# Optimization experiments

Measured on AMD Instinct MI355X. Metric: run time of the kernel, lower is better.

## Reference

```python
import jax, jax.numpy as jnp
import numpy as np
from jax import lax

B, P, DMAX, DMEL, H = 32, 192, 48, 80, 64
BN_EPS = 1e-5


def setup_inputs() -> dict:
    key = jax.random.key(0)
    ks = jax.random.split(key, 20)
    T = P * DMAX
    s = 0.1
    k_gru = 1.0 / np.sqrt(H)
    inp = {
        "mels": jax.random.normal(ks[0], (B, T, DMEL), jnp.float32),
        # phone durations in frames, in [1, DMAX]
        "durations": jax.random.randint(ks[1], (B, P), 0, DMAX, dtype=jnp.int32) + 1,
        "max_dur": DMAX,
        "conv_w": 1.0 + s * jax.random.normal(ks[2], (2,), jnp.float32),
        "conv_b": s * jax.random.normal(ks[3], (2,), jnp.float32),
        "bn_gamma": 0.5 + jax.random.uniform(ks[4], (2,), jnp.float32),
        "bn_beta": s * jax.random.normal(ks[5], (2,), jnp.float32),
        "bn_mean": s * jax.random.normal(ks[6], (2,), jnp.float32),
        "bn_var": 0.5 + jax.random.uniform(ks[7], (2,), jnp.float32),
        "W_ih_f": k_gru * jax.random.normal(ks[8], (3 * H, DMEL), jnp.float32),
        "W_hh_f": k_gru * jax.random.normal(ks[9], (3 * H, H), jnp.float32),
        "b_ih_f": k_gru * jax.random.normal(ks[10], (3 * H,), jnp.float32),
        "b_hh_f": k_gru * jax.random.normal(ks[11], (3 * H,), jnp.float32),
        "W_ih_b": k_gru * jax.random.normal(ks[12], (3 * H, DMEL), jnp.float32),
        "W_hh_b": k_gru * jax.random.normal(ks[13], (3 * H, H), jnp.float32),
        "b_ih_b": k_gru * jax.random.normal(ks[14], (3 * H,), jnp.float32),
        "b_hh_b": k_gru * jax.random.normal(ks[15], (3 * H,), jnp.float32),
    }
    return inp


def gru_cell(x, h, Wih, Whh, bih, bhh):
    # PyTorch GRU cell convention (gate order r, z, n)
    gi = x @ Wih.T + bih
    gh = h @ Whh.T + bhh
    ir, iz, inn = jnp.split(gi, 3, axis=-1)
    hr, hz, hn = jnp.split(gh, 3, axis=-1)
    r = jax.nn.sigmoid(ir + hr)
    z = jax.nn.sigmoid(iz + hz)
    n = jnp.tanh(inn + r * hn)
    return (1.0 - z) * n + z * h


def reference(mels, durations, max_dur, conv_w, conv_b, bn_gamma, bn_beta,
              bn_mean, bn_var, W_ih_f, W_hh_f, b_ih_f, b_hh_f,
              W_ih_b, W_hh_b, b_ih_b, b_hh_b):
    Bq, T, D = mels.shape
    Pq = durations.shape[1]
    Hq = W_hh_f.shape[1]

    # --- mel2phone: gather each phone's mel segment into [B, P, DMAX, D] ---
    ends = jnp.cumsum(durations, axis=1)
    starts = ends - durations
    t = jnp.arange(max_dur)
    idx = jnp.clip(starts[:, :, None] + t[None, None, :], 0, T - 1)  # [B,P,Dmax]
    segs = mels[jnp.arange(Bq)[:, None, None], idx]                  # [B,P,Dmax,D]
    mask = t[None, None, :] < durations[:, :, None]                  # [B,P,Dmax]

    # --- ConvBNorms2d: 1x1 single-channel conv + eval-mode BN + ReLU, x n_layers ---
    x = segs
    for i in range(conv_w.shape[0]):
        x = conv_w[i] * x + conv_b[i]
        x = (x - bn_mean[i]) * (bn_gamma[i] / jnp.sqrt(bn_var[i] + BN_EPS)) + bn_beta[i]
        x = jax.nn.relu(x)

    # --- per-segment bidirectional GRU, keep last valid timestep ---
    BP = Bq * Pq
    xs = x.reshape(BP, max_dur, D).transpose(1, 0, 2)        # [Dmax, BP, D]
    ms = mask.reshape(BP, max_dur).T                         # [Dmax, BP]

    def step(h, inp):
        xt, mt = inp
        hn = gru_cell(xt, h, W_ih_f, W_hh_f, b_ih_f, b_hh_f)
        h = jnp.where(mt[:, None], hn, h)  # freeze hidden past segment end
        return h, None

    h0 = jnp.zeros((BP, Hq), x.dtype)
    h_fwd, _ = lax.scan(step, h0, (xs, ms))                  # fwd hidden at len-1

    # backward direction output at the last valid position = one GRU step on x[len-1]
    last_idx = jnp.clip(durations - 1, 0, max_dur - 1)       # [B,P]
    x_last = jnp.take_along_axis(x, last_idx[:, :, None, None], axis=2)[:, :, 0, :]
    h_bwd = gru_cell(x_last.reshape(BP, D), h0, W_ih_b, W_hh_b, b_ih_b, b_hh_b)

    out = jnp.concatenate([h_fwd, h_bwd], axis=-1).reshape(Bq, Pq, 2 * Hq)
    out = out * (durations > 0)[:, :, None]  # phone2utter zero-padding
    return out


if __name__ == "__main__":
    o = reference(**setup_inputs())
    print(o.shape, o.dtype)
```

## Files before the change

### kernel.cpp

```cpp
#include <hip/hip_runtime.h>

#define NB 32
#define NP 192
#define DM 48
#define ND 80
#define NH 64
#define NT (NP*DM)
#define NBP (NB*NP)
#define NSG (NBP/16)

typedef _Float16 half8 __attribute__((ext_vector_type(8)));
typedef float f32x4 __attribute__((ext_vector_type(4)));

#define WS_STARTS 0
#define WS_WIH   32768
#define WS_WHH   (32768 + 36864)
#define WS_WIHB  (32768 + 36864 + 24576)

__device__ __forceinline__ float sigm(float x){ return 1.0f/(1.0f + __expf(-x)); }
__device__ __forceinline__ float tanh_f(float x){ return 1.0f - 2.0f/(1.0f + __expf(2.0f*x)); }

__device__ __forceinline__ unsigned packh2(float a, float b){
    unsigned short ua = __builtin_bit_cast(unsigned short, (_Float16)a);
    unsigned short ub = __builtin_bit_cast(unsigned short, (_Float16)b);
    return (unsigned)ua | ((unsigned)ub << 16);
}

struct Aff { float a0,c0,a1,c1; };
__device__ __forceinline__ Aff make_aff(const float* cw, const float* cb, const float* bg,
                                        const float* bb, const float* bm, const float* bv){
    float s0 = bg[0]*rsqrtf(bv[0]+1e-5f);
    float s1 = bg[1]*rsqrtf(bv[1]+1e-5f);
    Aff A;
    A.a0 = cw[0]*s0; A.c0 = (cb[0]-bm[0])*s0 + bb[0];
    A.a1 = cw[1]*s1; A.c1 = (cb[1]-bm[1])*s1 + bb[1];
    return A;
}
__device__ __forceinline__ float aff(float x, const Aff A){
    float y = fmaxf(fmaf(A.a0, x, A.c0), 0.0f);
    return fmaxf(fmaf(A.a1, y, A.c1), 0.0f);
}

__global__ __launch_bounds__(NP) void k_starts(const int* __restrict__ dur,
                                               int* __restrict__ starts){
    __shared__ int s[NP];
    int b = blockIdx.x, p = threadIdx.x;
    int d = dur[b*NP + p];
    s[p] = d;
    __syncthreads();
    #pragma unroll
    for (int off = 1; off < NP; off <<= 1){
        int v = (p >= off) ? s[p - off] : 0;
        __syncthreads();
        s[p] += v;
        __syncthreads();
    }
    starts[b*NP + p] = s[p] - d;
}

__global__ __launch_bounds__(256) void k_prep(const float* __restrict__ Wih,
                                              const float* __restrict__ Whh,
                                              const float* __restrict__ Wihb,
                                              unsigned short* __restrict__ wih16,
                                              unsigned short* __restrict__ whh16,
                                              unsigned short* __restrict__ wihb16){
    int idx = blockIdx.x*256 + threadIdx.x;
    if (idx < 12*3*64*8){
        int i = idx & 7, l = (idx>>3) & 63, ks = (idx>>9) % 3, f = idx / 1536;
        int j = (f>>2)*64 + (f&3)*16 + (l&15);
        int k = ks*32 + (l>>4)*8 + i;
        float v = (k < ND) ? Wih[j*ND + k] : 0.0f;
        wih16[idx] = __builtin_bit_cast(unsigned short, (_Float16)v);
        return;
    }
    int idx2 = idx - 12*3*64*8;
    if (idx2 < 12*2*64*8){
        int i = idx2 & 7, l = (idx2>>3) & 63, ks = (idx2>>9) & 1, f = idx2 / 1024;
        int j = (f>>2)*64 + (f&3)*16 + (l&15);
        int k = ks*32 + (l>>4)*8 + i;
        whh16[idx2] = __builtin_bit_cast(unsigned short, (_Float16)Whh[j*NH + k]);
        return;
    }
    int idx3 = idx2 - 12*2*64*8;
    if (idx3 < 12*3*64*8){
        int i = idx3 & 7, l = (idx3>>3) & 63, ks = (idx3>>9) % 3, f = idx3 / 1536;
        int j = (f>>2)*64 + (f&3)*16 + (l&15);
        int k = ks*32 + (l>>4)*8 + i;
        float v = (k < ND) ? Wihb[j*ND + k] : 0.0f;
        wihb16[idx3] = __builtin_bit_cast(unsigned short, (_Float16)v);
    }
}

__global__ __launch_bounds__(256, 2) void k_fused(
        const float* __restrict__ mels,
        const int* __restrict__ starts,
        const int* __restrict__ dur,
        const unsigned short* __restrict__ wih16,
        const unsigned short* __restrict__ whh16,
        const unsigned short* __restrict__ wihb16,
        const float* __restrict__ bih,  const float* __restrict__ bhh,
        const float* __restrict__ bihb, const float* __restrict__ bhhb,
        const float* __restrict__ cw, const float* __restrict__ cb,
        const float* __restrict__ bg, const float* __restrict__ bb,
        const float* __restrict__ bm, const float* __restrict__ bv,
        float* __restrict__ out){
    __shared__ alignas(16) unsigned short xh3[3*16*104];
    __shared__ alignas(16) unsigned short xl3[3*16*104];
    __shared__ alignas(16) unsigned short hh2[2*16*72];
    __shared__ alignas(16) unsigned short hl2[2*16*72];
    __shared__ alignas(16) float xlast[16*100];

    int sg  = blockIdx.x;
    int tid = threadIdx.x;
    int w = tid >> 6, l = tid & 63;
    int sc = l & 15, g4 = l >> 4;
    int b = sg / 12;
    Aff A = make_aff(cw,cb,bg,bb,bm,bv);

    half8 Af[3][3], Ah[3][2];
    #pragma unroll
    for (int gt = 0; gt < 3; ++gt){
        #pragma unroll
        for (int ks = 0; ks < 3; ++ks)
            Af[gt][ks] = *(const half8*)(wih16 + (size_t)(((gt*4+w)*3 + ks)*64 + l)*8);
        #pragma unroll
        for (int ks = 0; ks < 2; ++ks)
            Ah[gt][ks] = *(const half8*)(whh16 + (size_t)(((gt*4+w)*2 + ks)*64 + l)*8);
    }
    f32x4 bi[3], bh[3];
    #pragma unroll
    for (int gt = 0; gt < 3; ++gt){
        float4 t4 = *(const float4*)(bih + gt*64 + w*16 + g4*4);
        bi[gt][0]=t4.x; bi[gt][1]=t4.y; bi[gt][2]=t4.z; bi[gt][3]=t4.w;
        float4 u4 = *(const float4*)(bhh + gt*64 + w*16 + g4*4);
        bh[gt][0]=u4.x; bh[gt][1]=u4.y; bh[gt][2]=u4.z; bh[gt][3]=u4.w;
    }
    int dl_g = dur[sg*16 + sc];

    int s0 = tid/20, q0 = tid%20;
    bool has1 = ((tid & 3) == 0);
    int u1 = 256 + (tid >> 2);
    int s1 = u1/20, q1 = u1%20;
    int st0 = starts[sg*16 + s0], dl0 = dur[sg*16 + s0];
    int st1 = 0, dl1 = 0;
    if (has1){ st1 = starts[sg*16 + s1]; dl1 = dur[sg*16 + s1]; }
    const float* mb = mels + (size_t)b*NT*ND;

    auto ldx = [&](int st, int t, int q) -> float4 {
        int r = st + t; r = (r < NT-1) ? r : (NT-1);
        return *(const float4*)(mb + (size_t)r*ND + 4*q);
    };
    auto wrx = [&](int pw, int s, int q, float4 v, bool islast){
        float y0=aff(v.x,A), y1=aff(v.y,A), y2=aff(v.z,A), y3=aff(v.w,A);
        float p0=(float)(_Float16)y0, p1=(float)(_Float16)y1;
        float p2=(float)(_Float16)y2, p3=(float)(_Float16)y3;
        *(uint2*)&xh3[(pw*16+s)*104 + 4*q] = uint2{packh2(y0,y1), packh2(y2,y3)};
        *(uint2*)&xl3[(pw*16+s)*104 + 4*q] = uint2{packh2(y0-p0,y1-p1), packh2(y2-p2,y3-p3)};
        if (islast) *(float4*)&xlast[s*100 + 4*q] = make_float4(y0,y1,y2,y3);
    };

    for (int i = tid; i < 48; i += 256){
        int bf = i/16, s = i%16;
        *(uint4*)&xh3[(bf*16+s)*104 + 80] = uint4{0,0,0,0};
        *(uint4*)&xh3[(bf*16+s)*104 + 88] = uint4{0,0,0,0};
        *(uint4*)&xl3[(bf*16+s)*104 + 80] = uint4{0,0,0,0};
        *(uint4*)&xl3[(bf*16+s)*104 + 88] = uint4{0,0,0,0};
    }
    for (int i = tid; i < 80; i += 256){
        int s = i/5, c = i%5;
        *(float4*)&xlast[s*100 + 80 + 4*c] = make_float4(0,0,0,0);
    }
    for (int i = tid; i < 144; i += 256){
        int s = i/9, u = i%9;
        *(uint4*)&hh2[s*72 + u*8] = uint4{0,0,0,0};
        *(uint4*)&hl2[s*72 + u*8] = uint4{0,0,0,0};
    }

    {
        float4 v0 = ldx(st0, 0, q0);
        wrx(0, s0, q0, v0, (0 == dl0-1));
        if (has1){ float4 v1 = ldx(st1, 0, q1); wrx(0, s1, q1, v1, (0 == dl1-1)); }
    }
    float4 r0a = ldx(st0, 1, q0);
    float4 r0b = {0,0,0,0};
    if (has1) r0b = ldx(st1, 1, q1);
    float4 r1a = {0,0,0,0}, r1b = {0,0,0,0};
    float h[4] = {0.f,0.f,0.f,0.f};
    __syncthreads();

#define GSTEP(K, WA, WB, LA, LB)                                                      \
{                                                                                     \
    const int PR = (K) % 3, PW = ((K)+1) % 3, HB = (K) & 1;                           \
    int t = tb + (K);                                                                 \
    half8 Xh0 = *(const half8*)&xh3[(PR*16+sc)*104 +  0 + g4*8];                      \
    half8 Xh1 = *(const half8*)&xh3[(PR*16+sc)*104 + 32 + g4*8];                      \
    half8 Xh2 = *(const half8*)&xh3[(PR*16+sc)*104 + 64 + g4*8];                      \
    half8 Xl0 = *(const half8*)&xl3[(PR*16+sc)*104 +  0 + g4*8];                      \
    half8 Xl1 = *(const half8*)&xl3[(PR*16+sc)*104 + 32 + g4*8];                      \
    half8 Xl2 = *(const half8*)&xl3[(PR*16+sc)*104 + 64 + g4*8];                      \
    half8 Hh0 = *(const half8*)&hh2[(HB*16+sc)*72 +  0 + g4*8];                       \
    half8 Hh1 = *(const half8*)&hh2[(HB*16+sc)*72 + 32 + g4*8];                       \
    half8 Hl0 = *(const half8*)&hl2[(HB*16+sc)*72 +  0 + g4*8];                       \
    half8 Hl1 = *(const half8*)&hl2[(HB*16+sc)*72 + 32 + g4*8];                       \
    if (t+1 < DM){                                                                    \
        wrx(PW, s0, q0, WA, (t+1) == (dl0-1));                                        \
        if (has1) wrx(PW, s1, q1, WB, (t+1) == (dl1-1));                              \
    }                                                                                 \
    { int tn = (t+2 < DM) ? t+2 : DM-1;                                               \
      LA = ldx(st0, tn, q0);                                                          \
      if (has1) LB = ldx(st1, tn, q1); }                                              \
    f32x4 ga0 = bi[0], ga1 = bi[1], ga2 = bi[2];                                      \
    f32x4 ha0 = bh[0], ha1 = bh[1], ha2 = bh[2];                                      \
    ga0 = __builtin_amdgcn_mfma_f32_16x16x32_f16(Af[0][0], Xh0, ga0, 0,0,0);          \
    ga1 = __builtin_amdgcn_mfma_f32_16x16x32_f16(Af[1][0], Xh0, ga1, 0,0,0);          \
    ga2 = __builtin_amdgcn_mfma_f32_16x16x32_f16(Af[2][0], Xh0, ga2, 0,0,0);          \
    ha0 = __builtin_amdgcn_mfma_f32_16x16x32_f16(Ah[0][0], Hh0, ha0, 0,0,0);          \
    ha1 = __builtin_amdgcn_mfma_f32_16x16x32_f16(Ah[1][0], Hh0, ha1, 0,0,0);          \
    ha2 = __builtin_amdgcn_mfma_f32_16x16x32_f16(Ah[2][0], Hh0, ha2, 0,0,0);          \
    ga0 = __builtin_amdgcn_mfma_f32_16x16x32_f16(Af[0][0], Xl0, ga0, 0,0,0);          \
    ga1 = __builtin_amdgcn_mfma_f32_16x16x32_f16(Af[1][0], Xl0, ga1, 0,0,0);          \
    ga2 = __builtin_amdgcn_mfma_f32_16x16x32_f16(Af[2][0], Xl0, ga2, 0,0,0);          \
    ha0 = __builtin_amdgcn_mfma_f32_16x16x32_f16(Ah[0][0], Hl0, ha0, 0,0,0);          \
    ha1 = __builtin_amdgcn_mfma_f32_16x16x32_f16(Ah[1][0], Hl0, ha1, 0,0,0);          \
    ha2 = __builtin_amdgcn_mfma_f32_16x16x32_f16(Ah[2][0], Hl0, ha2, 0,0,0);          \
    ga0 = __builtin_amdgcn_mfma_f32_16x16x32_f16(Af[0][1], Xh1, ga0, 0,0,0);          \
    ga1 = __builtin_amdgcn_mfma_f32_16x16x32_f16(Af[1][1], Xh1, ga1, 0,0,0);          \
    ga2 = __builtin_amdgcn_mfma_f32_16x16x32_f16(Af[2][1], Xh1, ga2, 0,0,0);          \
    ha0 = __builtin_amdgcn_mfma_f32_16x16x32_f16(Ah[0][1], Hh1, ha0, 0,0,0);          \
    ha1 = __builtin_amdgcn_mfma_f32_16x16x32_f16(Ah[1][1], Hh1, ha1, 0,0,0);          \
    ha2 = __builtin_amdgcn_mfma_f32_16x16x32_f16(Ah[2][1], Hh1, ha2, 0,0,0);          \
    ga0 = __builtin_amdgcn_mfma_f32_16x16x32_f16(Af[0][1], Xl1, ga0, 0,0,0);          \
    ga1 = __builtin_amdgcn_mfma_f32_16x16x32_f16(Af[1][1], Xl1, ga1, 0,0,0);          \
    ga2 = __builtin_amdgcn_mfma_f32_16x16x32_f16(Af[2][1], Xl1, ga2, 0,0,0);          \
    ha0 = __builtin_amdgcn_mfma_f32_16x16x32_f16(Ah[0][1], Hl1, ha0, 0,0,0);          \
    ha1 = __builtin_amdgcn_mfma_f32_16x16x32_f16(Ah[1][1], Hl1, ha1, 0,0,0);          \
    ha2 = __builtin_amdgcn_mfma_f32_16x16x32_f16(Ah[2][1], Hl1, ha2, 0,0,0);          \
    ga0 = __builtin_amdgcn_mfma_f32_16x16x32_f16(Af[0][2], Xh2, ga0, 0,0,0);          \
    ga1 = __builtin_amdgcn_mfma_f32_16x16x32_f16(Af[1][2], Xh2, ga1, 0,0,0);          \
    ga2 = __builtin_amdgcn_mfma_f32_16x16x32_f16(Af[2][2], Xh2, ga2, 0,0,0);          \
    ga0 = __builtin_amdgcn_mfma_f32_16x16x32_f16(Af[0][2], Xl2, ga0, 0,0,0);          \
    ga1 = __builtin_amdgcn_mfma_f32_16x16x32_f16(Af[1][2], Xl2, ga1, 0,0,0);          \
    ga2 = __builtin_amdgcn_mfma_f32_16x16x32_f16(Af[2][2], Xl2, ga2, 0,0,0);          \
    _Pragma("unroll")                                                                 \
    for (int r = 0; r < 4; ++r){                                                      \
        float rr = sigm(ga0[r] + ha0[r]);                                             \
        float zz = sigm(ga1[r] + ha1[r]);                                             \
        float nn = tanh_f(ga2[r] + rr*ha2[r]);                                        \
        float hn2 = (1.0f - zz)*nn + zz*h[r];                                         \
        h[r] = (t < dl_g) ? hn2 : h[r];                                               \
    }                                                                                 \
    { float e0 = h[0]-(float)(_Float16)h[0], e1 = h[1]-(float)(_Float16)h[1];         \
      float e2 = h[2]-(float)(_Float16)h[2], e3 = h[3]-(float)(_Float16)h[3];         \
      *(uint2*)&hh2[((HB^1)*16+sc)*72 + w*16 + g4*4] =                                \
          uint2{packh2(h[0],h[1]), packh2(h[2],h[3])};                                \
      *(uint2*)&hl2[((HB^1)*16+sc)*72 + w*16 + g4*4] =                                \
          uint2{packh2(e0,e1), packh2(e2,e3)};                                        \
    }                                                                                 \
    __syncthreads();                                                                  \
}

    for (int tb = 0; tb < DM; tb += 6){
        GSTEP(0, r0a, r0b, r1a, r1b)
        GSTEP(1, r1a, r1b, r0a, r0b)
        GSTEP(2, r0a, r0b, r1a, r1b)
        GSTEP(3, r1a, r1b, r0a, r0b)
        GSTEP(4, r0a, r0b, r1a, r1b)
        GSTEP(5, r1a, r1b, r0a, r0b)
    }
#undef GSTEP

    float mk = (dl_g > 0) ? 1.0f : 0.0f;
    {
        float4 o4 = {h[0]*mk, h[1]*mk, h[2]*mk, h[3]*mk};
        *(float4*)(out + ((size_t)sg*16 + sc)*(2*NH) + w*16 + g4*4) = o4;
    }

    half8 Afb[3][3];
    #pragma unroll
    for (int gt = 0; gt < 3; ++gt)
        #pragma unroll
        for (int ks = 0; ks < 3; ++ks)
            Afb[gt][ks] = *(const half8*)(wihb16 + (size_t)(((gt*4+w)*3 + ks)*64 + l)*8);
    f32x4 ab0, ab1, ab2;
    {
        float4 t0 = *(const float4*)(bihb + 0*64 + w*16 + g4*4);
        float4 t1 = *(const float4*)(bihb + 1*64 + w*16 + g4*4);
        float4 t2 = *(const float4*)(bihb + 2*64 + w*16 + g4*4);
        ab0[0]=t0.x; ab0[1]=t0.y; ab0[2]=t0.z; ab0[3]=t0.w;
        ab1[0]=t1.x; ab1[1]=t1.y; ab1[2]=t1.z; ab1[3]=t1.w;
        ab2[0]=t2.x; ab2[1]=t2.y; ab2[2]=t2.z; ab2[3]=t2.w;
    }
    #pragma unroll
    for (int ks = 0; ks < 3; ++ks){
        float4 xa = *(const float4*)&xlast[sc*100 + ks*32 + g4*8];
        float4 xb = *(const float4*)&xlast[sc*100 + ks*32 + g4*8 + 4];
        float xv[8] = {xa.x,xa.y,xa.z,xa.w, xb.x,xb.y,xb.z,xb.w};
        half8 Bh, Bl;
        #pragma unroll
        for (int i = 0; i < 8; ++i){
            _Float16 hi = (_Float16)xv[i];
            Bh[i] = hi;
            Bl[i] = (_Float16)(xv[i] - (float)hi);
        }
        ab0 = __builtin_amdgcn_mfma_f32_16x16x32_f16(Afb[0][ks], Bh, ab0, 0,0,0);
        ab1 = __builtin_amdgcn_mfma_f32_16x16x32_f16(Afb[1][ks], Bh, ab1, 0,0,0);
        ab2 = __builtin_amdgcn_mfma_f32_16x16x32_f16(Afb[2][ks], Bh, ab2, 0,0,0);
        ab0 = __builtin_amdgcn_mfma_f32_16x16x32_f16(Afb[0][ks], Bl, ab0, 0,0,0);
        ab1 = __builtin_amdgcn_mfma_f32_16x16x32_f16(Afb[1][ks], Bl, ab1, 0,0,0);
        ab2 = __builtin_amdgcn_mfma_f32_16x16x32_f16(Afb[2][ks], Bl, ab2, 0,0,0);
    }
    {
        float4 p0 = *(const float4*)(bhhb + 0*64 + w*16 + g4*4);
        float4 p1 = *(const float4*)(bhhb + 1*64 + w*16 + g4*4);
        float4 p2 = *(const float4*)(bhhb + 2*64 + w*16 + g4*4);
        float pr0[4] = {p0.x,p0.y,p0.z,p0.w};
        float pr1[4] = {p1.x,p1.y,p1.z,p1.w};
        float pr2[4] = {p2.x,p2.y,p2.z,p2.w};
        float ho[4];
        #pragma unroll
        for (int r = 0; r < 4; ++r){
            float rr = sigm(ab0[r] + pr0[r]);
            float zz = sigm(ab1[r] + pr1[r]);
            float nn = tanh_f(ab2[r] + rr*pr2[r]);
            ho[r] = (1.0f - zz)*nn * mk;
        }
        float4 o4 = {ho[0], ho[1], ho[2], ho[3]};
        *(float4*)(out + ((size_t)sg*16 + sc)*(2*NH) + NH + w*16 + g4*4) = o4;
    }
}

extern "C" void kernel_launch(void* const* d_in, const int* in_sizes, int n_in,
                              void* d_out, int out_size, void* d_ws, size_t ws_size,
                              hipStream_t stream){
    const float* mels = (const float*)d_in[0];
    const int*   dur  = (const int*)d_in[1];
    const float* cw = (const float*)d_in[3];
    const float* cb = (const float*)d_in[4];
    const float* bg = (const float*)d_in[5];
    const float* bb = (const float*)d_in[6];
    const float* bm = (const float*)d_in[7];
    const float* bv = (const float*)d_in[8];
    const float* Wihf = (const float*)d_in[9];
    const float* Whhf = (const float*)d_in[10];
    const float* bihf = (const float*)d_in[11];
    const float* bhhf = (const float*)d_in[12];
    const float* Wihb = (const float*)d_in[13];
    const float* bihb = (const float*)d_in[15];
    const float* bhhb = (const float*)d_in[16];
    float* out = (float*)d_out;

    int*            starts = (int*)((char*)d_ws + WS_STARTS);
    unsigned short* wih16  = (unsigned short*)((char*)d_ws + WS_WIH);
    unsigned short* whh16  = (unsigned short*)((char*)d_ws + WS_WHH);
    unsigned short* wihb16 = (unsigned short*)((char*)d_ws + WS_WIHB);

    k_starts<<<NB, NP, 0, stream>>>(dur, starts);
    k_prep<<<192, 256, 0, stream>>>(Wihf, Whhf, Wihb, wih16, whh16, wihb16);
    k_fused<<<NSG, 256, 0, stream>>>(mels, starts, dur, wih16, whh16, wihb16,
                                     bihf, bhhf, bihb, bhhb,
                                     cw, cb, bg, bb, bm, bv, out);
}
```

Baseline: 245.0 us.

## Drop fp16 split-precision for inputs and stage x in MFMA-native LDS layout

Input activations are now staged in shared memory as a single fp16 value instead of a hi/lo fp16 pair. This removes a third of the per-step MFMAs for the input projection and halves the x staging traffic. The staging buffer is laid out in the exact per-lane MFMA operand order, so each step reads one contiguous uint4 per lane. Only 192 threads load two float4s each instead of the old uneven split. The __syncthreads is replaced by a custom LDS-only wait plus s_barrier, and the recurrent hidden state keeps its hi/lo split. The trade-off is lower precision on the input projection, which raises accuracy risk against the fp32 reference.

Result: faster. 220.0 us (-10.2%).

```diff
diff --git a/kernel.cpp b/kernel.cpp
--- a/kernel.cpp
+++ b/kernel.cpp
@@ -39,6 +39,12 @@
 __device__ __forceinline__ float aff(float x, const Aff A){
     float y = fmaxf(fmaf(A.a0, x, A.c0), 0.0f);
     return fmaxf(fmaf(A.a1, y, A.c1), 0.0f);
+}
+
+__device__ __forceinline__ void lds_barrier(){
+    asm volatile("s_waitcnt lgkmcnt(0)" ::: "memory");
+    __builtin_amdgcn_s_barrier();
+    asm volatile("" ::: "memory");
 }
 
 __global__ __launch_bounds__(NP) void k_starts(const int* __restrict__ dur,
@@ -104,17 +110,15 @@
         const float* __restrict__ bg, const float* __restrict__ bb,
         const float* __restrict__ bm, const float* __restrict__ bv,
         float* __restrict__ out){
-    __shared__ alignas(16) unsigned short xh3[3*16*104];
-    __shared__ alignas(16) unsigned short xl3[3*16*104];
-    __shared__ alignas(16) unsigned short hh2[2*16*72];
-    __shared__ alignas(16) unsigned short hl2[2*16*72];
-    __shared__ alignas(16) float xlast[16*100];
+    __shared__ alignas(16) uint4 xf[3*192];
+    __shared__ alignas(16) uint4 xlast[192];
+    __shared__ alignas(16) unsigned short hh2[2*1152];
+    __shared__ alignas(16) unsigned short hl2[2*1152];
 
     int sg  = blockIdx.x;
     int tid = threadIdx.x;
     int w = tid >> 6, l = tid & 63;
     int sc = l & 15, g4 = l >> 4;
-    int b = sg / 12;
     Aff A = make_aff(cw,cb,bg,bb,bm,bv);
 
     half8 Af[3][3], Ah[3][2];
@@ -137,110 +141,77 @@
     }
     int dl_g = dur[sg*16 + sc];
 
-    int s0 = tid/20, q0 = tid%20;
-    bool has1 = ((tid & 3) == 0);
-    int u1 = 256 + (tid >> 2);
-    int s1 = u1/20, q1 = u1%20;
-    int st0 = starts[sg*16 + s0], dl0 = dur[sg*16 + s0];
-    int st1 = 0, dl1 = 0;
-    if (has1){ st1 = starts[sg*16 + s1]; dl1 = dur[sg*16 + s1]; }
-    const float* mb = mels + (size_t)b*NT*ND;
-
-    auto ldx = [&](int st, int t, int q) -> float4 {
-        int r = st + t; r = (r < NT-1) ? r : (NT-1);
-        return *(const float4*)(mb + (size_t)r*ND + 4*q);
+    bool stg = (tid < 192);
+    int ks_s = tid >> 6, ls = tid & 63;
+    int scs = ls & 15, g4s = ls >> 4;
+    int k0 = ks_s*32 + g4s*8;
+    bool valid = stg && (k0 < ND);
+    int st_s = 0, d_s = -1;
+    if (stg){ st_s = starts[sg*16 + scs]; d_s = dur[sg*16 + scs]; }
+    const float* mb = mels + (size_t)(sg/12)*NT*ND;
+
+    auto ld2 = [&](int t, float4& va, float4& vb){
+        int r = st_s + t; r = (r < NT-1) ? r : (NT-1);
+        const float* p = mb + (size_t)r*ND + k0;
+        va = *(const float4*)p;
+        vb = *(const float4*)(p + 4);
     };
-    auto wrx = [&](int pw, int s, int q, float4 v, bool islast){
-        float y0=aff(v.x,A), y1=aff(v.y,A), y2=aff(v.z,A), y3=aff(v.w,A);
-        float p0=(float)(_Float16)y0, p1=(float)(_Float16)y1;
-        float p2=(float)(_Float16)y2, p3=(float)(_Float16)y3;
-        *(uint2*)&xh3[(pw*16+s)*104 + 4*q] = uint2{packh2(y0,y1), packh2(y2,y3)};
-        *(uint2*)&xl3[(pw*16+s)*104 + 4*q] = uint2{packh2(y0-p0,y1-p1), packh2(y2-p2,y3-p3)};
-        if (islast) *(float4*)&xlast[s*100 + 4*q] = make_float4(y0,y1,y2,y3);
+    auto stage = [&](int pw, int tt, float4 va, float4 vb){
+        if (valid){
+            float y0=aff(va.x,A), y1=aff(va.y,A), y2=aff(va.z,A), y3=aff(va.w,A);
+            float y4=aff(vb.x,A), y5=aff(vb.y,A), y6=aff(vb.z,A), y7=aff(vb.w,A);
+            uint4 P = uint4{packh2(y0,y1), packh2(y2,y3), packh2(y4,y5), packh2(y6,y7)};
+            xf[pw*192 + tid] = P;
+            if (tt == d_s - 1) xlast[tid] = P;
+        }
     };
 
-    for (int i = tid; i < 48; i += 256){
-        int bf = i/16, s = i%16;
-        *(uint4*)&xh3[(bf*16+s)*104 + 80] = uint4{0,0,0,0};
-        *(uint4*)&xh3[(bf*16+s)*104 + 88] = uint4{0,0,0,0};
-        *(uint4*)&xl3[(bf*16+s)*104 + 80] = uint4{0,0,0,0};
-        *(uint4*)&xl3[(bf*16+s)*104 + 88] = uint4{0,0,0,0};
-    }
-    for (int i = tid; i < 80; i += 256){
-        int s = i/5, c = i%5;
-        *(float4*)&xlast[s*100 + 80 + 4*c] = make_float4(0,0,0,0);
-    }
-    for (int i = tid; i < 144; i += 256){
-        int s = i/9, u = i%9;
-        *(uint4*)&hh2[s*72 + u*8] = uint4{0,0,0,0};
-        *(uint4*)&hl2[s*72 + u*8] = uint4{0,0,0,0};
-    }
-
-    {
-        float4 v0 = ldx(st0, 0, q0);
-        wrx(0, s0, q0, v0, (0 == dl0-1));
-        if (has1){ float4 v1 = ldx(st1, 0, q1); wrx(0, s1, q1, v1, (0 == dl1-1)); }
-    }
-    float4 r0a = ldx(st0, 1, q0);
-    float4 r0b = {0,0,0,0};
-    if (has1) r0b = ldx(st1, 1, q1);
-    float4 r1a = {0,0,0,0}, r1b = {0,0,0,0};
+    if (stg && !valid){
+        uint4 z = uint4{0,0,0,0};
+        xf[0*192 + tid] = z; xf[1*192 + tid] = z; xf[2*192 + tid] = z;
+        xlast[tid] = z;
+    }
+    for (int i = tid; i < 288; i += 256){
+        ((uint4*)hh2)[i] = uint4{0,0,0,0};
+        ((uint4*)hl2)[i] = uint4{0,0,0,0};
+    }
+    float4 va0 = {0,0,0,0}, vb0 = {0,0,0,0}, va1 = {0,0,0,0}, vb1 = {0,0,0,0};
+    if (valid) ld2(0, va0, vb0);
+    stage(0, 0, va0, vb0);
+    if (valid) ld2(1, va0, vb0);
     float h[4] = {0.f,0.f,0.f,0.f};
-    __syncthreads();
-
-#define GSTEP(K, WA, WB, LA, LB)                                                      \
+    lds_barrier();
+
+#define MFMA(a,b,c) __builtin_amdgcn_mfma_f32_16x16x32_f16(a,b,c,0,0,0)
+#define GSTEP(K, SA, SB, LA, LB)                                                      \
 {                                                                                     \
     const int PR = (K) % 3, PW = ((K)+1) % 3, HB = (K) & 1;                           \
-    int t = tb + (K);                                                                 \
-    half8 Xh0 = *(const half8*)&xh3[(PR*16+sc)*104 +  0 + g4*8];                      \
-    half8 Xh1 = *(const half8*)&xh3[(PR*16+sc)*104 + 32 + g4*8];                      \
-    half8 Xh2 = *(const half8*)&xh3[(PR*16+sc)*104 + 64 + g4*8];                      \
-    half8 Xl0 = *(const half8*)&xl3[(PR*16+sc)*104 +  0 + g4*8];                      \
-    half8 Xl1 = *(const half8*)&xl3[(PR*16+sc)*104 + 32 + g4*8];                      \
-    half8 Xl2 = *(const half8*)&xl3[(PR*16+sc)*104 + 64 + g4*8];                      \
-    half8 Hh0 = *(const half8*)&hh2[(HB*16+sc)*72 +  0 + g4*8];                       \
-    half8 Hh1 = *(const half8*)&hh2[(HB*16+sc)*72 + 32 + g4*8];                       \
-    half8 Hl0 = *(const half8*)&hl2[(HB*16+sc)*72 +  0 + g4*8];                       \
-    half8 Hl1 = *(const half8*)&hl2[(HB*16+sc)*72 + 32 + g4*8];                       \
-    if (t+1 < DM){                                                                    \
-        wrx(PW, s0, q0, WA, (t+1) == (dl0-1));                                        \
-        if (has1) wrx(PW, s1, q1, WB, (t+1) == (dl1-1));                              \
-    }                                                                                 \
-    { int tn = (t+2 < DM) ? t+2 : DM-1;                                               \
-      LA = ldx(st0, tn, q0);                                                          \
-      if (has1) LB = ldx(st1, tn, q1); }                                              \
+    const int t = tb + (K);                                                           \
+    half8 X0  = *(const half8*)&xf[PR*192 +   0 + l];                                 \
+    half8 X1  = *(const half8*)&xf[PR*192 +  64 + l];                                 \
+    half8 X2  = *(const half8*)&xf[PR*192 + 128 + l];                                 \
+    half8 Hh0 = *(const half8*)&hh2[HB*1152 + sc*72 +  0 + g4*8];                     \
+    half8 Hh1 = *(const half8*)&hh2[HB*1152 + sc*72 + 32 + g4*8];                     \
+    half8 Hl0 = *(const half8*)&hl2[HB*1152 + sc*72 +  0 + g4*8];                     \
+    half8 Hl1 = *(const half8*)&hl2[HB*1152 + sc*72 + 32 + g4*8];                     \
+    if (t+1 < DM) stage(PW, t+1, SA, SB);                                             \
+    if (valid && (t+2 < DM)) ld2(t+2, LA, LB);                                        \
     f32x4 ga0 = bi[0], ga1 = bi[1], ga2 = bi[2];                                      \
     f32x4 ha0 = bh[0], ha1 = bh[1], ha2 = bh[2];                                      \
-    ga0 = __builtin_amdgcn_mfma_f32_16x16x32_f16(Af[0][0], Xh0, ga0, 0,0,0);          \
-    ga1 = __builtin_amdgcn_mfma_f32_16x16x32_f16(Af[1][0], Xh0, ga1, 0,0,0);          \
-    ga2 = __builtin_amdgcn_mfma_f32_16x16x32_f16(Af[2][0], Xh0, ga2, 0,0,0);          \
-    ha0 = __builtin_amdgcn_mfma_f32_16x16x32_f16(Ah[0][0], Hh0, ha0, 0,0,0);          \
-    ha1 = __builtin_amdgcn_mfma_f32_16x16x32_f16(Ah[1][0], Hh0, ha1, 0,0,0);          \
-    ha2 = __builtin_amdgcn_mfma_f32_16x16x32_f16(Ah[2][0], Hh0, ha2, 0,0,0);          \
-    ga0 = __builtin_amdgcn_mfma_f32_16x16x32_f16(Af[0][0], Xl0, ga0, 0,0,0);          \
-    ga1 = __builtin_amdgcn_mfma_f32_16x16x32_f16(Af[1][0], Xl0, ga1, 0,0,0);          \
-    ga2 = __builtin_amdgcn_mfma_f32_16x16x32_f16(Af[2][0], Xl0, ga2, 0,0,0);          \
-    ha0 = __builtin_amdgcn_mfma_f32_16x16x32_f16(Ah[0][0], Hl0, ha0, 0,0,0);          \
-    ha1 = __builtin_amdgcn_mfma_f32_16x16x32_f16(Ah[1][0], Hl0, ha1, 0,0,0);          \
-    ha2 = __builtin_amdgcn_mfma_f32_16x16x32_f16(Ah[2][0], Hl0, ha2, 0,0,0);          \
-    ga0 = __builtin_amdgcn_mfma_f32_16x16x32_f16(Af[0][1], Xh1, ga0, 0,0,0);          \
-    ga1 = __builtin_amdgcn_mfma_f32_16x16x32_f16(Af[1][1], Xh1, ga1, 0,0,0);          \
-    ga2 = __builtin_amdgcn_mfma_f32_16x16x32_f16(Af[2][1], Xh1, ga2, 0,0,0);          \
-    ha0 = __builtin_amdgcn_mfma_f32_16x16x32_f16(Ah[0][1], Hh1, ha0, 0,0,0);          \
-    ha1 = __builtin_amdgcn_mfma_f32_16x16x32_f16(Ah[1][1], Hh1, ha1, 0,0,0);          \
-    ha2 = __builtin_amdgcn_mfma_f32_16x16x32_f16(Ah[2][1], Hh1, ha2, 0,0,0);          \
-    ga0 = __builtin_amdgcn_mfma_f32_16x16x32_f16(Af[0][1], Xl1, ga0, 0,0,0);          \
-    ga1 = __builtin_amdgcn_mfma_f32_16x16x32_f16(Af[1][1], Xl1, ga1, 0,0,0);          \
-    ga2 = __builtin_amdgcn_mfma_f32_16x16x32_f16(Af[2][1], Xl1, ga2, 0,0,0);          \
-    ha0 = __builtin_amdgcn_mfma_f32_16x16x32_f16(Ah[0][1], Hl1, ha0, 0,0,0);          \
-    ha1 = __builtin_amdgcn_mfma_f32_16x16x32_f16(Ah[1][1], Hl1, ha1, 0,0,0);          \
-    ha2 = __builtin_amdgcn_mfma_f32_16x16x32_f16(Ah[2][1], Hl1, ha2, 0,0,0);          \
-    ga0 = __builtin_amdgcn_mfma_f32_16x16x32_f16(Af[0][2], Xh2, ga0, 0,0,0);          \
-    ga1 = __builtin_amdgcn_mfma_f32_16x16x32_f16(Af[1][2], Xh2, ga1, 0,0,0);          \
-    ga2 = __builtin_amdgcn_mfma_f32_16x16x32_f16(Af[2][2], Xh2, ga2, 0,0,0);          \
-    ga0 = __builtin_amdgcn_mfma_f32_16x16x32_f16(Af[0][2], Xl2, ga0, 0,0,0);          \
-    ga1 = __builtin_amdgcn_mfma_f32_16x16x32_f16(Af[1][2], Xl2, ga1, 0,0,0);          \
-    ga2 = __builtin_amdgcn_mfma_f32_16x16x32_f16(Af[2][2], Xl2, ga2, 0,0,0);          \
+    ha0 = MFMA(Ah[0][0], Hh0, ha0); ha1 = MFMA(Ah[1][0], Hh0, ha1);                   \
+    ha2 = MFMA(Ah[2][0], Hh0, ha2);                                                   \
+    ga0 = MFMA(Af[0][0], X0, ga0);  ga1 = MFMA(Af[1][0], X0, ga1);                    \
+    ga2 = MFMA(Af[2][0], X0, ga2);                                                    \
+    ha0 = MFMA(Ah[0][0], Hl0, ha0); ha1 = MFMA(Ah[1][0], Hl0, ha1);                   \
+    ha2 = MFMA(Ah[2][0], Hl0, ha2);                                                   \
+    ga0 = MFMA(Af[0][1], X1, ga0);  ga1 = MFMA(Af[1][1], X1, ga1);                    \
+    ga2 = MFMA(Af[2][1], X1, ga2);                                                    \
+    ha0 = MFMA(Ah[0][1], Hh1, ha0); ha1 = MFMA(Ah[1][1], Hh1, ha1);                   \
+    ha2 = MFMA(Ah[2][1], Hh1, ha2);                                                   \
+    ha0 = MFMA(Ah[0][1], Hl1, ha0); ha1 = MFMA(Ah[1][1], Hl1, ha1);                   \
+    ha2 = MFMA(Ah[2][1], Hl1, ha2);                                                   \
+    ga0 = MFMA(Af[0][2], X2, ga0);  ga1 = MFMA(Af[1][2], X2, ga1);                    \
+    ga2 = MFMA(Af[2][2], X2, ga2);                                                    \
     _Pragma("unroll")                                                                 \
     for (int r = 0; r < 4; ++r){                                                      \
         float rr = sigm(ga0[r] + ha0[r]);                                             \
@@ -251,21 +222,21 @@
     }                                                                                 \
     { float e0 = h[0]-(float)(_Float16)h[0], e1 = h[1]-(float)(_Float16)h[1];         \
       float e2 = h[2]-(float)(_Float16)h[2], e3 = h[3]-(float)(_Float16)h[3];         \
-      *(uint2*)&hh2[((HB^1)*16+sc)*72 + w*16 + g4*4] =                                \
+      *(uint2*)&hh2[(HB^1)*1152 + sc*72 + w*16 + g4*4] =                              \
           uint2{packh2(h[0],h[1]), packh2(h[2],h[3])};                                \
-      *(uint2*)&hl2[((HB^1)*16+sc)*72 + w*16 + g4*4] =                                \
+      *(uint2*)&hl2[(HB^1)*1152 + sc*72 + w*16 + g4*4] =                              \
           uint2{packh2(e0,e1), packh2(e2,e3)};                                        \
     }                                                                                 \
-    __syncthreads();                                                                  \
+    lds_barrier();                                                                    \
 }
 
     for (int tb = 0; tb < DM; tb += 6){
-        GSTEP(0, r0a, r0b, r1a, r1b)
-        GSTEP(1, r1a, r1b, r0a, r0b)
-        GSTEP(2, r0a, r0b, r1a, r1b)
-        GSTEP(3, r1a, r1b, r0a, r0b)
-        GSTEP(4, r0a, r0b, r1a, r1b)
-        GSTEP(5, r1a, r1b, r0a, r0b)
+        GSTEP(0, va0, vb0, va1, vb1)
+        GSTEP(1, va1, vb1, va0, vb0)
+        GSTEP(2, va0, vb0, va1, vb1)
+        GSTEP(3, va1, vb1, va0, vb0)
+        GSTEP(4, va0, vb0, va1, vb1)
+        GSTEP(5, va1, vb1, va0, vb0)
     }
 #undef GSTEP
 
@@ -292,22 +263,10 @@
     }
     #pragma unroll
     for (int ks = 0; ks < 3; ++ks){
-        float4 xa = *(const float4*)&xlast[sc*100 + ks*32 + g4*8];
-        float4 xb = *(const float4*)&xlast[sc*100 + ks*32 + g4*8 + 4];
-        float xv[8] = {xa.x,xa.y,xa.z,xa.w, xb.x,xb.y,xb.z,xb.w};
-        half8 Bh, Bl;
-        #pragma unroll
-        for (int i = 0; i < 8; ++i){
-            _Float16 hi = (_Float16)xv[i];
-            Bh[i] = hi;
-            Bl[i] = (_Float16)(xv[i] - (float)hi);
-        }
-        ab0 = __builtin_amdgcn_mfma_f32_16x16x32_f16(Afb[0][ks], Bh, ab0, 0,0,0);
-        ab1 = __builtin_amdgcn_mfma_f32_16x16x32_f16(Afb[1][ks], Bh, ab1, 0,0,0);
-        ab2 = __builtin_amdgcn_mfma_f32_16x16x32_f16(Afb[2][ks], Bh, ab2, 0,0,0);
-        ab0 = __builtin_amdgcn_mfma_f32_16x16x32_f16(Afb[0][ks], Bl, ab0, 0,0,0);
-        ab1 = __builtin_amdgcn_mfma_f32_16x16x32_f16(Afb[1][ks], Bl, ab1, 0,0,0);
-        ab2 = __builtin_amdgcn_mfma_f32_16x16x32_f16(Afb[2][ks], Bl, ab2, 0,0,0);
+        half8 Bx = *(const half8*)&xlast[ks*64 + l];
+        ab0 = MFMA(Afb[0][ks], Bx, ab0);
+        ab1 = MFMA(Afb[1][ks], Bx, ab1);
+        ab2 = MFMA(Afb[2][ks], Bx, ab2);
     }
     {
         float4 p0 = *(const float4*)(bhhb + 0*64 + w*16 + g4*4);
@@ -327,6 +286,7 @@
         float4 o4 = {ho[0], ho[1], ho[2], ho[3]};
         *(float4*)(out + ((size_t)sg*16 + sc)*(2*NH) + NH + w*16 + g4*4) = o4;
     }
+#undef MFMA
 }
 
 extern "C" void kernel_launch(void* const* d_in, const int* in_sizes, int n_in,
```
